# Kernel optimization log

Measured on AMD Instinct MI355X. Metric: run time of the kernel, lower is better.

## Reference

```python
import jax, jax.numpy as jnp
import numpy as np

EMBED = 1024
HEADS = 16
HEAD_DIM = EMBED // HEADS
B, T = 1, 4096


def setup_inputs() -> dict:
    key = jax.random.key(0)
    k1, k2, k3, k4, k5 = jax.random.split(key, 5)
    scale = 1.0 / np.sqrt(EMBED)
    x = jax.random.normal(k1, (B, T, EMBED), dtype=jnp.float32)
    W_qkv = jax.random.normal(k2, (EMBED, 3 * EMBED), dtype=jnp.float32) * scale
    b_qkv = jax.random.normal(k3, (3 * EMBED,), dtype=jnp.float32) * 0.01
    W_out = jax.random.normal(k4, (EMBED, EMBED), dtype=jnp.float32) * scale
    b_out = jax.random.normal(k5, (EMBED,), dtype=jnp.float32) * 0.01
    return {"x": x, "W_qkv": W_qkv, "b_qkv": b_qkv, "W_out": W_out, "b_out": b_out}


def reference(x, W_qkv, b_qkv, W_out, b_out):
    Bn, Tn, C = x.shape
    qkv = x @ W_qkv + b_qkv                          # [B,T,3C]
    qkv = qkv.reshape(Bn, Tn, 3, HEADS, HEAD_DIM)
    qkv = jnp.transpose(qkv, (2, 0, 3, 1, 4))        # [3,B,H,T,hd]
    q, k, v = qkv[0], qkv[1], qkv[2]
    scores = jnp.einsum('bhqd,bhkd->bhqk', q, k) / jnp.sqrt(jnp.float32(HEAD_DIM))
    causal = jnp.tril(jnp.ones((Tn, Tn), dtype=bool))
    scores = jnp.where(causal, scores, -jnp.inf)
    attn = jax.nn.softmax(scores, axis=-1)
    out = jnp.einsum('bhqk,bhkd->bhqd', attn, v)     # [B,H,T,hd]
    out = jnp.transpose(out, (0, 2, 1, 3)).reshape(Bn, Tn, C)
    return out @ W_out + b_out
```

## Files before the change

kernel.cpp:

```cpp
#include <hip/hip_runtime.h>
#include <hip/hip_bf16.h>
#include <math.h>

#define EMBED 1024
#define HEADS 16
#define HDIM 64
#define T_SEQ 4096

typedef __bf16 bf16;
typedef bf16 bf16x8 __attribute__((ext_vector_type(8)));
typedef float f32x4 __attribute__((ext_vector_type(4)));
typedef float f32x16 __attribute__((ext_vector_type(16)));

__global__ __launch_bounds__(256) void f32_to_bf16(
    const float* __restrict__ in, bf16* __restrict__ out, int n) {
  int i = (blockIdx.x * 256 + threadIdx.x) * 8;
  if (i >= n) return;
  float4 a = *(const float4*)&in[i];
  float4 b = *(const float4*)&in[i + 4];
  bf16x8 o;
  o[0] = (bf16)a.x; o[1] = (bf16)a.y; o[2] = (bf16)a.z; o[3] = (bf16)a.w;
  o[4] = (bf16)b.x; o[5] = (bf16)b.y; o[6] = (bf16)b.z; o[7] = (bf16)b.w;
  *(bf16x8*)&out[i] = o;
}

__global__ __launch_bounds__(256) void transpose_f32_bf16(
    const float* __restrict__ in, bf16* __restrict__ out, int rows, int cols) {
  __shared__ bf16 t[32][33];
  const int c0 = blockIdx.x * 32, r0 = blockIdx.y * 32;
  const int tx = threadIdx.x & 31, ty = threadIdx.x >> 5;
#pragma unroll
  for (int i = 0; i < 4; ++i)
    t[ty + 8 * i][tx] = (bf16)in[(size_t)(r0 + ty + 8 * i) * cols + c0 + tx];
  __syncthreads();
#pragma unroll
  for (int i = 0; i < 4; ++i)
    out[(size_t)(c0 + ty + 8 * i) * rows + r0 + tx] = t[tx][ty + 8 * i];
}

__global__ __launch_bounds__(256) void transpose_v(
    const bf16* __restrict__ qkvb, bf16* __restrict__ vT) {
  __shared__ bf16 t[64][65];
  const int h = blockIdx.y;
  const int t0 = blockIdx.x * 64;
  const int tx = threadIdx.x & 63, ty = threadIdx.x >> 6;
#pragma unroll
  for (int i = 0; i < 16; ++i)
    t[ty + 4 * i][tx] =
        qkvb[(size_t)(t0 + ty + 4 * i) * (3 * EMBED) + 2 * EMBED + h * HDIM + tx];
  __syncthreads();
#pragma unroll
  for (int i = 0; i < 16; ++i)
    vT[((size_t)h * HDIM + ty + 4 * i) * T_SEQ + t0 + tx] = t[tx][ty + 4 * i];
}

template <bool OUT_F32>
__global__ __launch_bounds__(256) void gemm_bt_bias(
    const bf16* __restrict__ A, const bf16* __restrict__ BT,
    const float* __restrict__ bias, void* __restrict__ Cout,
    int M, int N, int K) {
  __shared__ __align__(16) bf16 As[128][40];
  __shared__ __align__(16) bf16 Bs[128][40];
  const int tid = threadIdx.x;
  const int lane = tid & 63;
  const int w = tid >> 6;
  const int wr = w >> 1, wc = w & 1;
  const int l16 = lane & 15, lq = lane >> 4;
  const int brow = blockIdx.y * 128;
  const int bcol = blockIdx.x * 128;

  f32x4 acc[4][4] = {};

  const int sr = tid >> 2;
  const int sc = (tid & 3) * 8;

  bf16x8 ra0, ra1, rb0, rb1;
#define LOAD_REGS(k0)                                                     \
  {                                                                       \
    ra0 = *(const bf16x8*)&A[(size_t)(brow + sr) * K + (k0) + sc];        \
    ra1 = *(const bf16x8*)&A[(size_t)(brow + sr + 64) * K + (k0) + sc];   \
    rb0 = *(const bf16x8*)&BT[(size_t)(bcol + sr) * K + (k0) + sc];       \
    rb1 = *(const bf16x8*)&BT[(size_t)(bcol + sr + 64) * K + (k0) + sc];  \
  }

  LOAD_REGS(0);
  for (int k0 = 0; k0 < K; k0 += 32) {
    __syncthreads();
    *(bf16x8*)&As[sr][sc] = ra0;
    *(bf16x8*)&As[sr + 64][sc] = ra1;
    *(bf16x8*)&Bs[sr][sc] = rb0;
    *(bf16x8*)&Bs[sr + 64][sc] = rb1;
    __syncthreads();
    if (k0 + 32 < K) LOAD_REGS(k0 + 32);

    bf16x8 af[4], bfr[4];
#pragma unroll
    for (int m = 0; m < 4; ++m)
      af[m] = *(const bf16x8*)&As[wr * 64 + m * 16 + l16][lq * 8];
#pragma unroll
    for (int n = 0; n < 4; ++n)
      bfr[n] = *(const bf16x8*)&Bs[wc * 64 + n * 16 + l16][lq * 8];
#pragma unroll
    for (int m = 0; m < 4; ++m)
#pragma unroll
      for (int n = 0; n < 4; ++n)
        acc[m][n] =
            __builtin_amdgcn_mfma_f32_16x16x32_bf16(af[m], bfr[n], acc[m][n], 0, 0, 0);
  }
#undef LOAD_REGS

#pragma unroll
  for (int m = 0; m < 4; ++m) {
    const int row = brow + wr * 64 + m * 16 + lq * 4;
#pragma unroll
    for (int n = 0; n < 4; ++n) {
      const int col = bcol + wc * 64 + n * 16 + l16;
      const float bv = bias[col];
#pragma unroll
      for (int r2 = 0; r2 < 4; ++r2) {
        float v = acc[m][n][r2] + bv;
        if (OUT_F32)
          ((float*)Cout)[(size_t)(row + r2) * N + col] = v;
        else
          ((bf16*)Cout)[(size_t)(row + r2) * N + col] = (bf16)v;
      }
    }
  }
}

__device__ __forceinline__ bf16x8 pk_swap8(float a0, float a1, float a2, float a3,
                                           float a4, float a5, float a6, float a7) {
  unsigned W0, W1, W2, W3;
  asm("v_cvt_pk_bf16_f32 %0, %1, %2" : "=v"(W0) : "v"(a0), "v"(a1));
  asm("v_cvt_pk_bf16_f32 %0, %1, %2" : "=v"(W1) : "v"(a2), "v"(a3));
  asm("v_cvt_pk_bf16_f32 %0, %1, %2" : "=v"(W2) : "v"(a4), "v"(a5));
  asm("v_cvt_pk_bf16_f32 %0, %1, %2" : "=v"(W3) : "v"(a6), "v"(a7));
  asm("v_permlane32_swap_b32 %0, %1" : "+v"(W0), "+v"(W2));
  asm("v_permlane32_swap_b32 %0, %1" : "+v"(W1), "+v"(W3));
  union { unsigned u[4]; bf16x8 v; } r;
  r.u[0] = W0; r.u[1] = W1; r.u[2] = W2; r.u[3] = W3;
  return r.v;
}

__global__ __launch_bounds__(256) void flash_attn_mfma(
    const bf16* __restrict__ qkvb, const bf16* __restrict__ vT,
    bf16* __restrict__ out, bf16* __restrict__ partO_main,
    bf16* __restrict__ partO_ovf, float2* __restrict__ partML) {
  const int h = blockIdx.y;
  const int job = 79 - (int)blockIdx.x;
  int qtb, np, part;
  if (job < 8)       { qtb = job;                np = 1; part = 0; }
  else if (job < 24) { qtb = 8 + ((job - 8) >> 1);  np = 2; part = (job - 8) & 1; }
  else if (job < 48) { int t = job - 24; qtb = 16 + t / 3; np = 3; part = t - (t / 3) * 3; }
  else               { int t = job - 48; qtb = 24 + (t >> 2); np = 4; part = t & 3; }
  const int nt = 2 * qtb + 2;
  const int bsz = nt / np, rem = nt % np;
  const int k0t = part * bsz + min(part, rem);
  const int k1t = k0t + bsz + (part < rem ? 1 : 0);

  int lslot = -1;
  if (np > 1) {
    if (qtb < 16)      lslot = (qtb - 8) * 2 + part;
    else if (qtb < 24) lslot = 16 + (qtb - 16) * 3 + part;
    else               lslot = 40 + (qtb - 24) * 4 + part;
  }

  const int q0 = qtb * 128;
  const int tid = threadIdx.x;
  const int lane = tid & 63;
  const int w = tid >> 6;
  const int qi = lane & 31;
  const int hi = lane >> 5;

  __shared__ __align__(16) bf16 Ks[64 * 64];
  __shared__ __align__(16) bf16 Vs[64 * 64];

  const int qrow = q0 + w * 32 + qi;

  bf16x8 qb0, qb1, qb2, qb3;
  {
    const bf16* qp = &qkvb[(size_t)qrow * (3 * EMBED) + h * HDIM + hi * 8];
    qb0 = *(const bf16x8*)(qp + 0);
    qb1 = *(const bf16x8*)(qp + 16);
    qb2 = *(const bf16x8*)(qp + 32);
    qb3 = *(const bf16x8*)(qp + 48);
#pragma unroll
    for (int j = 0; j < 8; ++j) {
      qb0[j] = (bf16)((float)qb0[j] * 0.125f);
      qb1[j] = (bf16)((float)qb1[j] * 0.125f);
      qb2[j] = (bf16)((float)qb2[j] * 0.125f);
      qb3[j] = (bf16)((float)qb3[j] * 0.125f);
    }
  }

  f32x16 oA = {}, oB = {};
  float m_r = -INFINITY, l_r = 0.f;

  const int strow = tid >> 3;
  const int stslot = tid & 7;

  bf16x8 rk0, rk1, rv0, rv1;
#define LOAD_KV(kt)                                                                 \
  {                                                                                 \
    rk0 = *(const bf16x8*)&qkvb[(size_t)((kt) * 64 + strow) * (3 * EMBED) + EMBED + \
                                h * HDIM + stslot * 8];                             \
    rk1 = *(const bf16x8*)&qkvb[(size_t)((kt) * 64 + strow + 32) * (3 * EMBED) +    \
                                EMBED + h * HDIM + stslot * 8];                     \
    rv0 = *(const bf16x8*)&vT[((size_t)h * HDIM + strow) * T_SEQ + (kt) * 64 +      \
                              stslot * 8];                                          \
    rv1 = *(const bf16x8*)&vT[((size_t)h * HDIM + strow + 32) * T_SEQ + (kt) * 64 + \
                              stslot * 8];                                          \
  }

  LOAD_KV(k0t);
  for (int kt = k0t; kt < k1t; ++kt) {
    __syncthreads();
    *(bf16x8*)&Ks[strow * 64 + ((stslot ^ (strow & 7)) << 3)] = rk0;
    *(bf16x8*)&Ks[(strow + 32) * 64 + ((stslot ^ (strow & 7)) << 3)] = rk1;
    *(bf16x8*)&Vs[strow * 64 + ((stslot ^ (strow & 7)) << 3)] = rv0;
    *(bf16x8*)&Vs[(strow + 32) * 64 + ((stslot ^ (strow & 7)) << 3)] = rv1;
    __syncthreads();
    if (kt + 1 < k1t) LOAD_KV(kt + 1);

    if (kt * 64 > q0 + w * 32 + 31) continue;

    f32x16 sA = {}, sB = {};
    __builtin_amdgcn_s_setprio(1);
#pragma unroll
    for (int c = 0; c < 4; ++c) {
      const int sl = ((2 * c + hi) ^ (qi & 7)) << 3;
      bf16x8 kfA = *(const bf16x8*)&Ks[qi * 64 + sl];
      bf16x8 kfB = *(const bf16x8*)&Ks[(qi + 32) * 64 + sl];
      bf16x8 qf = (c == 0) ? qb0 : (c == 1) ? qb1 : (c == 2) ? qb2 : qb3;
      sA = __builtin_amdgcn_mfma_f32_32x32x16_bf16(kfA, qf, sA, 0, 0, 0);
      sB = __builtin_amdgcn_mfma_f32_32x32x16_bf16(kfB, qf, sB, 0, 0, 0);
    }
    __builtin_amdgcn_s_setprio(0);

    if (kt * 64 + 63 > q0 + w * 32) {
      const int qg = qrow;
#pragma unroll
      for (int r = 0; r < 16; ++r) {
        const int kl = (r & 3) + 8 * (r >> 2) + 4 * hi;
        if (kt * 64 + kl > qg) sA[r] = -INFINITY;
        if (kt * 64 + 32 + kl > qg) sB[r] = -INFINITY;
      }
    }

    float tm[16];
#pragma unroll
    for (int r = 0; r < 16; ++r) tm[r] = fmaxf(sA[r], sB[r]);
#pragma unroll
    for (int s = 8; s >= 1; s >>= 1)
#pragma unroll
      for (int r = 0; r < s; ++r) tm[r] = fmaxf(tm[r], tm[r + s]);
    const float pm = fmaxf(tm[0], __shfl_xor(tm[0], 32));

    if (!__all(pm <= m_r + 8.f)) {
      const float mnew = fmaxf(m_r, pm);
      const float corr = __expf(m_r - mnew);
      l_r *= corr;
#pragma unroll
      for (int r = 0; r < 16; ++r) { oA[r] *= corr; oB[r] *= corr; }
      m_r = mnew;
    }

#pragma unroll
    for (int r = 0; r < 16; ++r) sA[r] = __expf(sA[r] - m_r);
#pragma unroll
    for (int r = 0; r < 16; ++r) sB[r] = __expf(sB[r] - m_r);

    float ts[16];
#pragma unroll
    for (int r = 0; r < 16; ++r) ts[r] = sA[r] + sB[r];
#pragma unroll
    for (int s = 8; s >= 1; s >>= 1)
#pragma unroll
      for (int r = 0; r < s; ++r) ts[r] += ts[r + s];
    l_r += ts[0];

    bf16x8 pf0 = pk_swap8(sA[0], sA[1], sA[2], sA[3], sA[4], sA[5], sA[6], sA[7]);
    bf16x8 pf1 = pk_swap8(sA[8], sA[9], sA[10], sA[11], sA[12], sA[13], sA[14], sA[15]);
    bf16x8 pf2 = pk_swap8(sB[0], sB[1], sB[2], sB[3], sB[4], sB[5], sB[6], sB[7]);
    bf16x8 pf3 = pk_swap8(sB[8], sB[9], sB[10], sB[11], sB[12], sB[13], sB[14], sB[15]);

    __builtin_amdgcn_s_setprio(1);
#pragma unroll
    for (int c = 0; c < 4; ++c) {
      const int sl = ((2 * c + hi) ^ (qi & 7)) << 3;
      bf16x8 vfA = *(const bf16x8*)&Vs[qi * 64 + sl];
      bf16x8 vfB = *(const bf16x8*)&Vs[(qi + 32) * 64 + sl];
      bf16x8 pf = (c == 0) ? pf0 : (c == 1) ? pf1 : (c == 2) ? pf2 : pf3;
      oA = __builtin_amdgcn_mfma_f32_32x32x16_bf16(vfA, pf, oA, 0, 0, 0);
      oB = __builtin_amdgcn_mfma_f32_32x32x16_bf16(vfB, pf, oB, 0, 0, 0);
    }
    __builtin_amdgcn_s_setprio(0);
  }
#undef LOAD_KV

  const float lt = l_r + __shfl_xor(l_r, 32);
  const float inv = lt > 0.f ? 1.f / lt : 0.f;
#pragma unroll
  for (int r = 0; r < 16; ++r) { oA[r] *= inv; oB[r] *= inv; }

  bf16x8 e0 = pk_swap8(oA[0], oA[1], oA[2], oA[3], oA[4], oA[5], oA[6], oA[7]);
  bf16x8 e1 = pk_swap8(oA[8], oA[9], oA[10], oA[11], oA[12], oA[13], oA[14], oA[15]);
  bf16x8 e2 = pk_swap8(oB[0], oB[1], oB[2], oB[3], oB[4], oB[5], oB[6], oB[7]);
  bf16x8 e3 = pk_swap8(oB[8], oB[9], oB[10], oB[11], oB[12], oB[13], oB[14], oB[15]);

  if (lslot < 0) {
    bf16* ob = &out[(size_t)qrow * EMBED + h * HDIM];
    *(bf16x8*)(ob + hi * 8) = e0;
    *(bf16x8*)(ob + 16 + hi * 8) = e1;
    *(bf16x8*)(ob + 32 + hi * 8) = e2;
    *(bf16x8*)(ob + 48 + hi * 8) = e3;
  } else {
    const int gslot = h * 72 + lslot;
    bf16* base = (gslot < 1024)
                     ? (bf16*)((char*)partO_main + (size_t)gslot * 16384)
                     : (bf16*)((char*)partO_ovf + (size_t)(gslot - 1024) * 16384);
    const int lr = w * 32 + qi;
    bf16* pb = base + (size_t)lr * 64;
    *(bf16x8*)(pb + hi * 8) = e0;
    *(bf16x8*)(pb + 16 + hi * 8) = e1;
    *(bf16x8*)(pb + 32 + hi * 8) = e2;
    *(bf16x8*)(pb + 48 + hi * 8) = e3;
    if (hi == 0) partML[gslot * 128 + lr] = make_float2(m_r, lt);
  }
}

__global__ __launch_bounds__(256) void merge_partials(
    const bf16* __restrict__ partO_main, const bf16* __restrict__ partO_ovf,
    const float2* __restrict__ partML, bf16* __restrict__ out) {
  const int qtb = 8 + blockIdx.x;
  const int h = blockIdx.y;
  int np, lbase;
  if (qtb < 16)      { np = 2; lbase = (qtb - 8) * 2; }
  else if (qtb < 24) { np = 3; lbase = 16 + (qtb - 16) * 3; }
  else               { np = 4; lbase = 40 + (qtb - 24) * 4; }
  const int gbase = h * 72 + lbase;
  const int r = threadIdx.x >> 1;
  const int dh = (threadIdx.x & 1) * 32;

  float mm = -INFINITY;
  float mv[4], lv[4];
#pragma unroll
  for (int p = 0; p < 4; ++p)
    if (p < np) {
      const float2 ml = partML[(gbase + p) * 128 + r];
      mv[p] = ml.x; lv[p] = ml.y;
      mm = fmaxf(mm, ml.x);
    }
  float wsum = 0.f, wgt[4];
#pragma unroll
  for (int p = 0; p < 4; ++p)
    if (p < np) {
      wgt[p] = lv[p] * __expf(mv[p] - mm);
      wsum += wgt[p];
    }
  const float inv = 1.f / wsum;
#pragma unroll
  for (int p = 0; p < 4; ++p)
    if (p < np) wgt[p] *= inv;

  const bf16* pp[4];
#pragma unroll
  for (int p = 0; p < 4; ++p)
    if (p < np) {
      const int gs = gbase + p;
      const bf16* base = (gs < 1024)
                             ? (const bf16*)((const char*)partO_main + (size_t)gs * 16384)
                             : (const bf16*)((const char*)partO_ovf + (size_t)(gs - 1024) * 16384);
      pp[p] = base + (size_t)r * 64 + dh;
    }

  bf16* ob = &out[(size_t)(qtb * 128 + r) * EMBED + h * HDIM + dh];
#pragma unroll
  for (int c = 0; c < 4; ++c) {
    float acc[8] = {0.f, 0.f, 0.f, 0.f, 0.f, 0.f, 0.f, 0.f};
#pragma unroll
    for (int p = 0; p < 4; ++p)
      if (p < np) {
        bf16x8 v = *(const bf16x8*)(pp[p] + c * 8);
#pragma unroll
        for (int j = 0; j < 8; ++j) acc[j] += wgt[p] * (float)v[j];
      }
    bf16x8 o;
#pragma unroll
    for (int j = 0; j < 8; ++j) o[j] = (bf16)acc[j];
    *(bf16x8*)(ob + c * 8) = o;
  }
}

extern "C" void kernel_launch(void* const* d_in, const int* in_sizes, int n_in,
                              void* d_out, int out_size, void* d_ws, size_t ws_size,
                              hipStream_t stream) {
  const float* x     = (const float*)d_in[0];
  const float* W_qkv = (const float*)d_in[1];
  const float* b_qkv = (const float*)d_in[2];
  const float* W_out = (const float*)d_in[3];
  const float* b_out = (const float*)d_in[4];
  float* out = (float*)d_out;

  char* ws = (char*)d_ws;
  const size_t MB = 1024 * 1024;
  bf16* x_bf   = (bf16*)(ws + 0);
  bf16* WqkvT  = (bf16*)(ws + 8 * MB);
  bf16* WoutT  = (bf16*)(ws + 14 * MB);
  bf16* qkvb   = (bf16*)(ws + 16 * MB);
  bf16* vT     = (bf16*)(ws + 40 * MB);
  bf16* attn_o = (bf16*)(ws + 48 * MB);
  bf16*   partO_main = (bf16*)d_out;
  bf16*   partO_ovf  = (bf16*)(ws + 0);
  float2* partML     = (float2*)(ws + 8 * MB);

  f32_to_bf16<<<(T_SEQ * EMBED) / (256 * 8), 256, 0, stream>>>(x, x_bf, T_SEQ * EMBED);
  transpose_f32_bf16<<<dim3(3 * EMBED / 32, EMBED / 32), 256, 0, stream>>>(
      W_qkv, WqkvT, EMBED, 3 * EMBED);
  transpose_f32_bf16<<<dim3(EMBED / 32, EMBED / 32), 256, 0, stream>>>(
      W_out, WoutT, EMBED, EMBED);

  gemm_bt_bias<false><<<dim3(3 * EMBED / 128, T_SEQ / 128), 256, 0, stream>>>(
      x_bf, WqkvT, b_qkv, qkvb, T_SEQ, 3 * EMBED, EMBED);

  transpose_v<<<dim3(T_SEQ / 64, HEADS), 256, 0, stream>>>(qkvb, vT);

  flash_attn_mfma<<<dim3(80, HEADS), 256, 0, stream>>>(qkvb, vT, attn_o, partO_main,
                                                       partO_ovf, partML);
  merge_partials<<<dim3(24, HEADS), 256, 0, stream>>>(partO_main, partO_ovf, partML,
                                                      attn_o);

  gemm_bt_bias<true><<<dim3(EMBED / 128, T_SEQ / 128), 256, 0, stream>>>(
      attn_o, WoutT, b_out, out, T_SEQ, EMBED, EMBED);
}
```

Before: 162.7 us.

## Stream GEMM and attention tiles into double-buffered LDS via global_load_lds, use exp2

Result: slower. 171.5 us (+5.4%).

```diff
diff --git a/kernel.cpp b/kernel.cpp
--- a/kernel.cpp
+++ b/kernel.cpp
@@ -11,6 +11,17 @@
 typedef bf16 bf16x8 __attribute__((ext_vector_type(8)));
 typedef float f32x4 __attribute__((ext_vector_type(4)));
 typedef float f32x16 __attribute__((ext_vector_type(16)));
+
+#define GL(gp, lp)                                                            \
+  __builtin_amdgcn_global_load_lds(                                           \
+      (const __attribute__((address_space(1))) void*)(gp),                    \
+      (__attribute__((address_space(3))) void*)(lp), 16, 0, 0)
+
+__device__ __forceinline__ float fexp2(float x) {
+  float r;
+  asm("v_exp_f32 %0, %1" : "=v"(r) : "v"(x));
+  return r;
+}
 
 __global__ __launch_bounds__(256) void f32_to_bf16(
     const float* __restrict__ in, bf16* __restrict__ out, int n) {
@@ -59,8 +70,8 @@
     const bf16* __restrict__ A, const bf16* __restrict__ BT,
     const float* __restrict__ bias, void* __restrict__ Cout,
     int M, int N, int K) {
-  __shared__ __align__(16) bf16 As[128][40];
-  __shared__ __align__(16) bf16 Bs[128][40];
+  __shared__ __align__(16) bf16 As[2][128 * 32];
+  __shared__ __align__(16) bf16 Bs[2][128 * 32];
   const int tid = threadIdx.x;
   const int lane = tid & 63;
   const int w = tid >> 6;
@@ -69,45 +80,44 @@
   const int brow = blockIdx.y * 128;
   const int bcol = blockIdx.x * 128;
 
+  const int strow = w * 32 + (lane >> 2);
+  const int stsl = (lane & 3) * 8;
+  const bf16* Abase = A + (size_t)(brow + strow) * K + stsl;
+  const bf16* Bbase = BT + (size_t)(bcol + strow) * K + stsl;
+
+#define STAGE_G(buf, k0)                                        \
+  {                                                             \
+    GL(Abase + (k0), &As[buf][(w * 32) * 32]);                  \
+    GL(Abase + (k0) + 16 * K, &As[buf][(w * 32 + 16) * 32]);    \
+    GL(Bbase + (k0), &Bs[buf][(w * 32) * 32]);                  \
+    GL(Bbase + (k0) + 16 * K, &Bs[buf][(w * 32 + 16) * 32]);    \
+  }
+
   f32x4 acc[4][4] = {};
 
-  const int sr = tid >> 2;
-  const int sc = (tid & 3) * 8;
-
-  bf16x8 ra0, ra1, rb0, rb1;
-#define LOAD_REGS(k0)                                                     \
-  {                                                                       \
-    ra0 = *(const bf16x8*)&A[(size_t)(brow + sr) * K + (k0) + sc];        \
-    ra1 = *(const bf16x8*)&A[(size_t)(brow + sr + 64) * K + (k0) + sc];   \
-    rb0 = *(const bf16x8*)&BT[(size_t)(bcol + sr) * K + (k0) + sc];       \
-    rb1 = *(const bf16x8*)&BT[(size_t)(bcol + sr + 64) * K + (k0) + sc];  \
-  }
-
-  LOAD_REGS(0);
-  for (int k0 = 0; k0 < K; k0 += 32) {
-    __syncthreads();
-    *(bf16x8*)&As[sr][sc] = ra0;
-    *(bf16x8*)&As[sr + 64][sc] = ra1;
-    *(bf16x8*)&Bs[sr][sc] = rb0;
-    *(bf16x8*)&Bs[sr + 64][sc] = rb1;
-    __syncthreads();
-    if (k0 + 32 < K) LOAD_REGS(k0 + 32);
+  STAGE_G(0, 0);
+  __syncthreads();
+  for (int k0 = 0, it = 0; k0 < K; k0 += 32, ++it) {
+    const int cur = it & 1;
+    if (k0 + 32 < K) STAGE_G(cur ^ 1, k0 + 32);
 
     bf16x8 af[4], bfr[4];
 #pragma unroll
     for (int m = 0; m < 4; ++m)
-      af[m] = *(const bf16x8*)&As[wr * 64 + m * 16 + l16][lq * 8];
+      af[m] = *(const bf16x8*)&As[cur][(wr * 64 + m * 16 + l16) * 32 + lq * 8];
 #pragma unroll
     for (int n = 0; n < 4; ++n)
-      bfr[n] = *(const bf16x8*)&Bs[wc * 64 + n * 16 + l16][lq * 8];
+      bfr[n] = *(const bf16x8*)&Bs[cur][(wc * 64 + n * 16 + l16) * 32 + lq * 8];
 #pragma unroll
     for (int m = 0; m < 4; ++m)
 #pragma unroll
       for (int n = 0; n < 4; ++n)
         acc[m][n] =
             __builtin_amdgcn_mfma_f32_16x16x32_bf16(af[m], bfr[n], acc[m][n], 0, 0, 0);
-  }
-#undef LOAD_REGS
+
+    __syncthreads();
+  }
+#undef STAGE_G
 
 #pragma unroll
   for (int m = 0; m < 4; ++m) {
@@ -172,11 +182,12 @@
   const int qi = lane & 31;
   const int hi = lane >> 5;
 
-  __shared__ __align__(16) bf16 Ks[64 * 64];
-  __shared__ __align__(16) bf16 Vs[64 * 64];
+  __shared__ __align__(16) bf16 Ks[2][64 * 64];
+  __shared__ __align__(16) bf16 Vs[2][64 * 64];
 
   const int qrow = q0 + w * 32 + qi;
 
+  const float QSCALE = 0.1803368867f;
   bf16x8 qb0, qb1, qb2, qb3;
   {
     const bf16* qp = &qkvb[(size_t)qrow * (3 * EMBED) + h * HDIM + hi * 8];
@@ -186,117 +197,114 @@
     qb3 = *(const bf16x8*)(qp + 48);
 #pragma unroll
     for (int j = 0; j < 8; ++j) {
-      qb0[j] = (bf16)((float)qb0[j] * 0.125f);
-      qb1[j] = (bf16)((float)qb1[j] * 0.125f);
-      qb2[j] = (bf16)((float)qb2[j] * 0.125f);
-      qb3[j] = (bf16)((float)qb3[j] * 0.125f);
+      qb0[j] = (bf16)((float)qb0[j] * QSCALE);
+      qb1[j] = (bf16)((float)qb1[j] * QSCALE);
+      qb2[j] = (bf16)((float)qb2[j] * QSCALE);
+      qb3[j] = (bf16)((float)qb3[j] * QSCALE);
     }
   }
 
   f32x16 oA = {}, oB = {};
   float m_r = -INFINITY, l_r = 0.f;
 
-  const int strow = tid >> 3;
-  const int stslot = tid & 7;
-
-  bf16x8 rk0, rk1, rv0, rv1;
-#define LOAD_KV(kt)                                                                 \
-  {                                                                                 \
-    rk0 = *(const bf16x8*)&qkvb[(size_t)((kt) * 64 + strow) * (3 * EMBED) + EMBED + \
-                                h * HDIM + stslot * 8];                             \
-    rk1 = *(const bf16x8*)&qkvb[(size_t)((kt) * 64 + strow + 32) * (3 * EMBED) +    \
-                                EMBED + h * HDIM + stslot * 8];                     \
-    rv0 = *(const bf16x8*)&vT[((size_t)h * HDIM + strow) * T_SEQ + (kt) * 64 +      \
-                              stslot * 8];                                          \
-    rv1 = *(const bf16x8*)&vT[((size_t)h * HDIM + strow + 32) * T_SEQ + (kt) * 64 + \
-                              stslot * 8];                                          \
-  }
-
-  LOAD_KV(k0t);
+  const int krow = lane >> 3;
+  const int ksl = ((lane & 7) ^ krow) * 8;
+  const bf16* Kbase =
+      qkvb + (size_t)(w * 16 + krow) * (3 * EMBED) + EMBED + h * HDIM + ksl;
+  const bf16* Vbase = vT + ((size_t)h * HDIM + w * 16 + krow) * T_SEQ + ksl;
+
+#define STAGE_KV(buf, kt)                                                      \
+  {                                                                            \
+    GL(Kbase + (size_t)(kt) * 64 * (3 * EMBED), &Ks[buf][(w * 16) * 64]);      \
+    GL(Kbase + (size_t)(kt) * 64 * (3 * EMBED) + (size_t)8 * (3 * EMBED),      \
+       &Ks[buf][(w * 16 + 8) * 64]);                                           \
+    GL(Vbase + (kt) * 64, &Vs[buf][(w * 16) * 64]);                            \
+    GL(Vbase + (kt) * 64 + 8 * T_SEQ, &Vs[buf][(w * 16 + 8) * 64]);            \
+  }
+
+  STAGE_KV(0, k0t);
+  __syncthreads();
   for (int kt = k0t; kt < k1t; ++kt) {
+    const int cur = (kt - k0t) & 1;
+    if (kt + 1 < k1t) STAGE_KV(cur ^ 1, kt + 1);
+
+    if (!(kt * 64 > q0 + w * 32 + 31)) {
+      f32x16 sA = {}, sB = {};
+      __builtin_amdgcn_s_setprio(1);
+#pragma unroll
+      for (int c = 0; c < 4; ++c) {
+        const int sl = ((2 * c + hi) ^ (qi & 7)) << 3;
+        bf16x8 kfA = *(const bf16x8*)&Ks[cur][qi * 64 + sl];
+        bf16x8 kfB = *(const bf16x8*)&Ks[cur][(qi + 32) * 64 + sl];
+        bf16x8 qf = (c == 0) ? qb0 : (c == 1) ? qb1 : (c == 2) ? qb2 : qb3;
+        sA = __builtin_amdgcn_mfma_f32_32x32x16_bf16(kfA, qf, sA, 0, 0, 0);
+        sB = __builtin_amdgcn_mfma_f32_32x32x16_bf16(kfB, qf, sB, 0, 0, 0);
+      }
+      __builtin_amdgcn_s_setprio(0);
+
+      if (kt * 64 + 63 > q0 + w * 32) {
+        const int qg = qrow;
+#pragma unroll
+        for (int r = 0; r < 16; ++r) {
+          const int kl = (r & 3) + 8 * (r >> 2) + 4 * hi;
+          if (kt * 64 + kl > qg) sA[r] = -INFINITY;
+          if (kt * 64 + 32 + kl > qg) sB[r] = -INFINITY;
+        }
+      }
+
+      float tm[16];
+#pragma unroll
+      for (int r = 0; r < 16; ++r) tm[r] = fmaxf(sA[r], sB[r]);
+#pragma unroll
+      for (int s = 8; s >= 1; s >>= 1)
+#pragma unroll
+        for (int r = 0; r < s; ++r) tm[r] = fmaxf(tm[r], tm[r + s]);
+      const float pm = fmaxf(tm[0], __shfl_xor(tm[0], 32));
+
+      if (!__all(pm <= m_r + 11.5416f)) {
+        const float mnew = fmaxf(m_r, pm);
+        const float corr = fexp2(m_r - mnew);
+        l_r *= corr;
+#pragma unroll
+        for (int r = 0; r < 16; ++r) { oA[r] *= corr; oB[r] *= corr; }
+        m_r = mnew;
+      }
+
+#pragma unroll
+      for (int r = 0; r < 16; ++r) sA[r] = fexp2(sA[r] - m_r);
+#pragma unroll
+      for (int r = 0; r < 16; ++r) sB[r] = fexp2(sB[r] - m_r);
+
+      float ts[16];
+#pragma unroll
+      for (int r = 0; r < 16; ++r) ts[r] = sA[r] + sB[r];
+#pragma unroll
+      for (int s = 8; s >= 1; s >>= 1)
+#pragma unroll
+        for (int r = 0; r < s; ++r) ts[r] += ts[r + s];
+      l_r += ts[0];
+
+      bf16x8 pf0 = pk_swap8(sA[0], sA[1], sA[2], sA[3], sA[4], sA[5], sA[6], sA[7]);
+      bf16x8 pf1 = pk_swap8(sA[8], sA[9], sA[10], sA[11], sA[12], sA[13], sA[14], sA[15]);
+      bf16x8 pf2 = pk_swap8(sB[0], sB[1], sB[2], sB[3], sB[4], sB[5], sB[6], sB[7]);
+      bf16x8 pf3 = pk_swap8(sB[8], sB[9], sB[10], sB[11], sB[12], sB[13], sB[14], sB[15]);
+
+      __builtin_amdgcn_s_setprio(1);
+#pragma unroll
+      for (int c = 0; c < 4; ++c) {
+        const int sl = ((2 * c + hi) ^ (qi & 7)) << 3;
+        bf16x8 vfA = *(const bf16x8*)&Vs[cur][qi * 64 + sl];
+        bf16x8 vfB = *(const bf16x8*)&Vs[cur][(qi + 32) * 64 + sl];
+        bf16x8 pf = (c == 0) ? pf0 : (c == 1) ? pf1 : (c == 2) ? pf2 : pf3;
+        oA = __builtin_amdgcn_mfma_f32_32x32x16_bf16(vfA, pf, oA, 0, 0, 0);
+        oB = __builtin_amdgcn_mfma_f32_32x32x16_bf16(vfB, pf, oB, 0, 0, 0);
+      }
+      __builtin_amdgcn_s_setprio(0);
+    }
+
     __syncthreads();
-    *(bf16x8*)&Ks[strow * 64 + ((stslot ^ (strow & 7)) << 3)] = rk0;
-    *(bf16x8*)&Ks[(strow + 32) * 64 + ((stslot ^ (strow & 7)) << 3)] = rk1;
-    *(bf16x8*)&Vs[strow * 64 + ((stslot ^ (strow & 7)) << 3)] = rv0;
-    *(bf16x8*)&Vs[(strow + 32) * 64 + ((stslot ^ (strow & 7)) << 3)] = rv1;
-    __syncthreads();
-    if (kt + 1 < k1t) LOAD_KV(kt + 1);
-
-    if (kt * 64 > q0 + w * 32 + 31) continue;
-
-    f32x16 sA = {}, sB = {};
-    __builtin_amdgcn_s_setprio(1);
-#pragma unroll
-    for (int c = 0; c < 4; ++c) {
-      const int sl = ((2 * c + hi) ^ (qi & 7)) << 3;
-      bf16x8 kfA = *(const bf16x8*)&Ks[qi * 64 + sl];
-      bf16x8 kfB = *(const bf16x8*)&Ks[(qi + 32) * 64 + sl];
-      bf16x8 qf = (c == 0) ? qb0 : (c == 1) ? qb1 : (c == 2) ? qb2 : qb3;
-      sA = __builtin_amdgcn_mfma_f32_32x32x16_bf16(kfA, qf, sA, 0, 0, 0);
-      sB = __builtin_amdgcn_mfma_f32_32x32x16_bf16(kfB, qf, sB, 0, 0, 0);
-    }
-    __builtin_amdgcn_s_setprio(0);
-
-    if (kt * 64 + 63 > q0 + w * 32) {
-      const int qg = qrow;
-#pragma unroll
-      for (int r = 0; r < 16; ++r) {
-        const int kl = (r & 3) + 8 * (r >> 2) + 4 * hi;
-        if (kt * 64 + kl > qg) sA[r] = -INFINITY;
-        if (kt * 64 + 32 + kl > qg) sB[r] = -INFINITY;
-      }
-    }
-
-    float tm[16];
-#pragma unroll
-    for (int r = 0; r < 16; ++r) tm[r] = fmaxf(sA[r], sB[r]);
-#pragma unroll
-    for (int s = 8; s >= 1; s >>= 1)
-#pragma unroll
-      for (int r = 0; r < s; ++r) tm[r] = fmaxf(tm[r], tm[r + s]);
-    const float pm = fmaxf(tm[0], __shfl_xor(tm[0], 32));
-
-    if (!__all(pm <= m_r + 8.f)) {
-      const float mnew = fmaxf(m_r, pm);
-      const float corr = __expf(m_r - mnew);
-      l_r *= corr;
-#pragma unroll
-      for (int r = 0; r < 16; ++r) { oA[r] *= corr; oB[r] *= corr; }
-      m_r = mnew;
-    }
-
-#pragma unroll
-    for (int r = 0; r < 16; ++r) sA[r] = __expf(sA[r] - m_r);
-#pragma unroll
-    for (int r = 0; r < 16; ++r) sB[r] = __expf(sB[r] - m_r);
-
-    float ts[16];
-#pragma unroll
-    for (int r = 0; r < 16; ++r) ts[r] = sA[r] + sB[r];
-#pragma unroll
-    for (int s = 8; s >= 1; s >>= 1)
-#pragma unroll
-      for (int r = 0; r < s; ++r) ts[r] += ts[r + s];
-    l_r += ts[0];
-
-    bf16x8 pf0 = pk_swap8(sA[0], sA[1], sA[2], sA[3], sA[4], sA[5], sA[6], sA[7]);
-    bf16x8 pf1 = pk_swap8(sA[8], sA[9], sA[10], sA[11], sA[12], sA[13], sA[14], sA[15]);
-    bf16x8 pf2 = pk_swap8(sB[0], sB[1], sB[2], sB[3], sB[4], sB[5], sB[6], sB[7]);
-    bf16x8 pf3 = pk_swap8(sB[8], sB[9], sB[10], sB[11], sB[12], sB[13], sB[14], sB[15]);
-
-    __builtin_amdgcn_s_setprio(1);
-#pragma unroll
-    for (int c = 0; c < 4; ++c) {
-      const int sl = ((2 * c + hi) ^ (qi & 7)) << 3;
-      bf16x8 vfA = *(const bf16x8*)&Vs[qi * 64 + sl];
-      bf16x8 vfB = *(const bf16x8*)&Vs[(qi + 32) * 64 + sl];
-      bf16x8 pf = (c == 0) ? pf0 : (c == 1) ? pf1 : (c == 2) ? pf2 : pf3;
-      oA = __builtin_amdgcn_mfma_f32_32x32x16_bf16(vfA, pf, oA, 0, 0, 0);
-      oB = __builtin_amdgcn_mfma_f32_32x32x16_bf16(vfB, pf, oB, 0, 0, 0);
-    }
-    __builtin_amdgcn_s_setprio(0);
-  }
-#undef LOAD_KV
+  }
+#undef STAGE_KV
 
   const float lt = l_r + __shfl_xor(l_r, 32);
   const float inv = lt > 0.f ? 1.f / lt : 0.f;
@@ -355,7 +363,7 @@
 #pragma unroll
   for (int p = 0; p < 4; ++p)
     if (p < np) {
-      wgt[p] = lv[p] * __expf(mv[p] - mm);
+      wgt[p] = lv[p] * fexp2(mv[p] - mm);
       wsum += wgt[p];
     }
   const float inv = 1.f / wsum;
```
